# Kernel tuning notes

Hardware: AMD Instinct MI355X
Metric: run time of the kernel (lower is better)

## Reference

```python
import jax, jax.numpy as jnp
import numpy as np

K_CHEB = 3  # Chebyshev order K -> K+1 basis matrices, gcn order = K


def setup_inputs() -> dict:
    key = jax.random.key(0)
    ks = jax.random.split(key, 7)
    B, N, T, Cin, Cout, ndim = 32, 512, 12, 64, 64, 40
    support_len = K_CHEB + 1
    cin_total = (K_CHEB * support_len + 1) * Cin  # (order*support_len+1)*c_in = 832
    x = jax.random.normal(ks[0], (B, N, T, Cin), jnp.float32)
    adj = (jax.random.uniform(ks[1], (N, N)) < 0.05).astype(jnp.float32)
    adjacency = jnp.maximum(adj, jnp.eye(N, dtype=jnp.float32))
    embedding = jax.random.uniform(ks[2], (N, ndim), dtype=jnp.float32)  # nn.init.uniform_
    W1 = jax.random.normal(ks[3], (ndim, ndim // 2), jnp.float32) * 0.3
    W2 = jax.random.normal(ks[4], (ndim, ndim // 2), jnp.float32) * 0.3
    mlp_w = jax.random.normal(ks[5], (Cout, cin_total), jnp.float32) / np.float32(np.sqrt(cin_total))
    mlp_b = jnp.zeros((Cout,), jnp.float32)
    return {"x": x, "adjacency": adjacency, "embedding": embedding,
            "W1": W1, "W2": W2, "mlp_w": mlp_w, "mlp_b": mlp_b}


def _cheb_kernels(adjacency, embedding, W1, W2):
    # adaptive adjacency: embedding mixed through column-softmaxed projections
    e1 = embedding @ jax.nn.softmax(W1, axis=0)
    e2 = embedding @ jax.nn.softmax(W2, axis=0)
    e1 = e1 / (jnp.linalg.norm(e1, axis=1, keepdims=True) + 1e-8)
    e2 = e2 / (jnp.linalg.norm(e2, axis=1, keepdims=True) + 1e-8)
    weight = e1 @ e2.T  # (N, N)
    A = jnp.where(adjacency > 0.0, weight + adjacency, jnp.asarray(9e-15, adjacency.dtype))
    # symmetric normalization: L = I - D^-1/2 A D^-1/2 ; Ls = (2/maxeig)*L - I with maxeig=2 -> Ls = -sym(A)
    d = 1.0 / jnp.sqrt(A.sum(axis=1))
    Ls = -(d[:, None] * A * d[None, :])
    I = jnp.eye(A.shape[0], dtype=A.dtype)
    kernels = [I, Ls]
    for _ in range(1, K_CHEB):  # Chebyshev recursion: T_{k+1} = 2 Ls T_k - T_{k-1}
        kernels.append(2.0 * (Ls @ kernels[-1]) - kernels[-2])
    return kernels  # K_CHEB + 1 matrices of (N, N)


def reference(x, adjacency, embedding, W1, W2, mlp_w, mlp_b):
    supports = _cheb_kernels(adjacency, embedding, W1, W2)
    xp = jnp.transpose(x, (0, 3, 1, 2))  # (B, Cin, N, T)
    out = [xp]
    for a in supports:
        x1 = jnp.einsum('bcvt,vw->bcwt', xp, a)
        out.append(x1)
        for _ in range(2, K_CHEB + 1):  # gcn order = K_CHEB
            x1 = jnp.einsum('bcvt,vw->bcwt', x1, a)
            out.append(x1)
    h = jnp.concatenate(out, axis=1)  # (B, 832, N, T)
    h = jnp.einsum('bcvt,oc->bovt', h, mlp_w) + mlp_b[None, :, None, None]  # 1x1 conv
    h = jnp.transpose(h, (0, 2, 3, 1))  # (B, N, T, Cout)
    return jax.nn.relu(h + x)  # conv_r is None (Cin == Cout), dropout eval no-op
```

## Files before the change

### kernel.cpp

```cpp
#include <hip/hip_runtime.h>
#include <hip/hip_bf16.h>

typedef unsigned short ushortT;
typedef unsigned int uintT;
typedef __attribute__((ext_vector_type(8))) short bf16x8;
typedef __attribute__((ext_vector_type(4))) float f32x4;
typedef __attribute__((ext_vector_type(4))) unsigned short us4;
typedef __attribute__((ext_vector_type(8))) unsigned short us8;

__device__ __forceinline__ ushortT f2bf(float f) {
    union { float f; uintT u; } x; x.f = f;
    uintT r = x.u + 0x7fffu + ((x.u >> 16) & 1u);
    return (ushortT)(r >> 16);
}
__device__ __forceinline__ float bf2f(ushortT u) {
    union { uintT u; float f; } x; x.u = ((uintT)u) << 16; return x.f;
}

#define ZLD 260
#define KTOT 5120

__global__ __launch_bounds__(256) void k_embed(const float* __restrict__ emb,
                                               const float* __restrict__ W1,
                                               const float* __restrict__ W2,
                                               float* __restrict__ e1,
                                               float* __restrict__ e2) {
    __shared__ float sW[800];
    __shared__ float sWs[800];
    const float* W = (blockIdx.x == 0) ? W1 : W2;
    float* e = (blockIdx.x == 0) ? e1 : e2;
    int tid = threadIdx.x;
    for (int i = tid; i < 800; i += 256) sW[i] = W[i];
    __syncthreads();
    if (tid < 20) {
        float mx = -1e30f;
        for (int i = 0; i < 40; ++i) mx = fmaxf(mx, sW[i * 20 + tid]);
        float s = 0.f;
        for (int i = 0; i < 40; ++i) s += __expf(sW[i * 20 + tid] - mx);
        float inv = 1.f / s;
        for (int i = 0; i < 40; ++i) sWs[i * 20 + tid] = __expf(sW[i * 20 + tid] - mx) * inv;
    }
    __syncthreads();
    for (int row = tid; row < 512; row += 256) {
        float acc[20];
        #pragma unroll
        for (int j = 0; j < 20; ++j) acc[j] = 0.f;
        for (int i = 0; i < 40; ++i) {
            float ev = emb[row * 40 + i];
            #pragma unroll
            for (int j = 0; j < 20; ++j) acc[j] += ev * sWs[i * 20 + j];
        }
        float s = 0.f;
        #pragma unroll
        for (int j = 0; j < 20; ++j) s += acc[j] * acc[j];
        float scale = 1.f / (sqrtf(s) + 1e-8f);
        #pragma unroll
        for (int j = 0; j < 20; ++j) e[row * 20 + j] = acc[j] * scale;
    }
}

__global__ __launch_bounds__(256) void k_adj(const float* __restrict__ adj,
                                             const float* __restrict__ e1,
                                             const float* __restrict__ e2,
                                             float* __restrict__ A,
                                             float* __restrict__ d) {
    int v = blockIdx.x, tid = threadIdx.x;
    __shared__ float ev[20];
    if (tid < 20) ev[tid] = e1[v * 20 + tid];
    __syncthreads();
    float local = 0.f;
    for (int w = tid; w < 512; w += 256) {
        float dot = 0.f;
        #pragma unroll
        for (int j = 0; j < 20; ++j) dot += ev[j] * e2[w * 20 + j];
        float av = adj[v * 512 + w];
        float Av = (av > 0.f) ? (dot + av) : 9e-15f;
        A[v * 512 + w] = Av;
        local += Av;
    }
    __shared__ float red[256];
    red[tid] = local;
    __syncthreads();
    for (int s = 128; s > 0; s >>= 1) {
        if (tid < s) red[tid] += red[tid + s];
        __syncthreads();
    }
    if (tid == 0) d[v] = 1.f / sqrtf(red[0]);
}

__global__ __launch_bounds__(256) void k_m(const float* __restrict__ A,
                                           const float* __restrict__ d,
                                           ushortT* __restrict__ P) {
    int w = blockIdx.x, tid = threadIdx.x;
    float dw = d[w];
    for (int v = tid; v < 512; v += 256) {
        float val = -d[v] * dw * A[v * 512 + w];
        P[512 * 512 + w * 512 + v] = f2bf(val);
        P[w * 512 + v] = (v == w) ? (ushortT)0x3F80 : (ushortT)0;
    }
}

__global__ __launch_bounds__(256) void k_w(const float* __restrict__ mlp_w,
                                           ushortT* __restrict__ Wq) {
    int idx = blockIdx.x * 256 + threadIdx.x;
    if (idx >= 10 * 64 * 64) return;
    int q = idx >> 12, rem = idx & 4095, o = rem >> 6, c = rem & 63;
    float v;
    if (q == 0) {
        v = 0.f;
        #pragma unroll
        for (int k = 0; k < 4; ++k) v += mlp_w[o * 832 + k * 64 + c];
    } else {
        v = mlp_w[o * 832 + (q + 3) * 64 + c];
    }
    Wq[idx] = f2bf(v);
}

__global__ __launch_bounds__(256) void k_gemm512(const ushortT* __restrict__ A,
                                                 const ushortT* __restrict__ B,
                                                 ushortT* __restrict__ out1,
                                                 ushortT* __restrict__ out2,
                                                 int mode,
                                                 const ushortT* __restrict__ aux,
                                                 const ushortT* __restrict__ A2,
                                                 const ushortT* __restrict__ B2,
                                                 ushortT* __restrict__ out3) {
    int bx = blockIdx.x;
    if (bx >= 64) { A = A2; B = B2; out1 = out3; out2 = nullptr; mode = 0; bx -= 64; }
    int wave = threadIdx.x >> 6, lane = threadIdx.x & 63;
    int lr = lane & 15, lg = lane >> 4;
    int mbase = (bx >> 3) * 64;
    int nbase = (bx & 7) * 64 + wave * 16;
    f32x4 acc[4] = {};
    for (int kk = 0; kk < 16; ++kk) {
        int k0 = kk * 32 + lg * 8;
        bf16x8 bfr;
        #pragma unroll
        for (int j = 0; j < 8; ++j) bfr[j] = (short)B[(k0 + j) * 512 + nbase + lr];
        #pragma unroll
        for (int wt = 0; wt < 4; ++wt) {
            bf16x8 af = *(const bf16x8*)(A + (mbase + wt * 16 + lr) * 512 + k0);
            acc[wt] = __builtin_amdgcn_mfma_f32_16x16x32_bf16(af, bfr, acc[wt], 0, 0, 0);
        }
    }
    #pragma unroll
    for (int wt = 0; wt < 4; ++wt)
        #pragma unroll
        for (int r = 0; r < 4; ++r) {
            int row = mbase + wt * 16 + lg * 4 + r;
            int col = nbase + lr;
            float v = acc[wt][r];
            out1[row * 512 + col] = f2bf(v);
            if (mode == 1) out2[row * 512 + col] = f2bf(2.f * v - (row == col ? 1.f : 0.f));
            else if (mode == 2) out2[row * 512 + col] = f2bf(4.f * v - 3.f * bf2f(aux[row * 512 + col]));
        }
}

__global__ __launch_bounds__(256) void k_z(const float* __restrict__ x,
                                           const ushortT* __restrict__ Wq,
                                           ushortT* __restrict__ Z,
                                           int slab0) {
    __shared__ ushortT Zl[64 * ZLD];
    int bid = blockIdx.x;
    int btl = bid >> 1, chunk = bid & 1;
    int bt = slab0 + btl;
    int b = bt / 12, t = bt - b * 12;
    int tid = threadIdx.x, wave = tid >> 6, lane = tid & 63;
    int lr = lane & 15, lg = lane >> 4;

    bf16x8 xn[4][2];
    const float* xb = x + ((size_t)b * 512 * 12 + t) * 64;
    #pragma unroll
    for (int vt = 0; vt < 4; ++vt) {
        int vrow = chunk * 256 + wave * 64 + vt * 16 + lr;
        const float* px = xb + (size_t)vrow * 768 + lg * 8;
        f32x4 f0 = *(const f32x4*)px;
        f32x4 f1 = *(const f32x4*)(px + 4);
        f32x4 f2 = *(const f32x4*)(px + 32);
        f32x4 f3 = *(const f32x4*)(px + 36);
        bf16x8 v0, v1;
        v0[0] = (short)f2bf(f0[0]); v0[1] = (short)f2bf(f0[1]);
        v0[2] = (short)f2bf(f0[2]); v0[3] = (short)f2bf(f0[3]);
        v0[4] = (short)f2bf(f1[0]); v0[5] = (short)f2bf(f1[1]);
        v0[6] = (short)f2bf(f1[2]); v0[7] = (short)f2bf(f1[3]);
        v1[0] = (short)f2bf(f2[0]); v1[1] = (short)f2bf(f2[1]);
        v1[2] = (short)f2bf(f2[2]); v1[3] = (short)f2bf(f2[3]);
        v1[4] = (short)f2bf(f3[0]); v1[5] = (short)f2bf(f3[1]);
        v1[6] = (short)f2bf(f3[2]); v1[7] = (short)f2bf(f3[3]);
        xn[vt][0] = v0;
        xn[vt][1] = v1;
    }

    #pragma unroll 1
    for (int q = 0; q < 10; ++q) {
        const ushortT* wqp = Wq + q * 4096;
        #pragma unroll
        for (int ot = 0; ot < 4; ++ot) {
            int o = ot * 16 + lr;
            bf16x8 wf0 = *(const bf16x8*)(wqp + o * 64 + lg * 8);
            bf16x8 wf1 = *(const bf16x8*)(wqp + o * 64 + 32 + lg * 8);
            #pragma unroll
            for (int vt = 0; vt < 4; ++vt) {
                f32x4 z = {};
                z = __builtin_amdgcn_mfma_f32_16x16x32_bf16(xn[vt][0], wf0, z, 0, 0, 0);
                z = __builtin_amdgcn_mfma_f32_16x16x32_bf16(xn[vt][1], wf1, z, 0, 0, 0);
                us4 pk = { f2bf(z[0]), f2bf(z[1]), f2bf(z[2]), f2bf(z[3]) };
                *(us4*)&Zl[o * ZLD + wave * 64 + vt * 16 + lg * 4] = pk;
            }
        }
        __syncthreads();
        size_t kbase = (size_t)q * 512 + chunk * 256;
        #pragma unroll
        for (int j = 0; j < 8; ++j) {
            int flat = j * 256 + tid;
            int o = flat >> 5, slot = flat & 31;
            us4 lo = *(const us4*)&Zl[o * ZLD + slot * 8];
            us4 hi = *(const us4*)&Zl[o * ZLD + slot * 8 + 4];
            us8 val = { lo[0], lo[1], lo[2], lo[3], hi[0], hi[1], hi[2], hi[3] };
            *(us8*)&Z[(size_t)(btl * 64 + o) * KTOT + kbase + slot * 8] = val;
        }
        __syncthreads();
    }
}

__global__ __launch_bounds__(256) void k_big(const ushortT* __restrict__ P,
                                             const ushortT* __restrict__ Z,
                                             const float* __restrict__ x,
                                             const float* __restrict__ bias,
                                             float* __restrict__ out,
                                             int slab0) {
    __shared__ ushortT SA[3][4096];
    __shared__ ushortT SB[3][4096];
    int nwg = (int)gridDim.x;
    int bid = (int)blockIdx.x;
    int cpx = nwg >> 3;
    int lbid = (bid & 7) * cpx + (bid >> 3);
    int mblk = lbid & 3;
    int nblk = lbid >> 2;
    int mbase = mblk * 128;
    int n0 = nblk * 128;
    int tid = threadIdx.x, wave = tid >> 6, lane = tid & 63;
    int lr = lane & 15, lg = lane >> 4;
    int wm = wave >> 1, wn = wave & 1;
    int srow = tid >> 2, sg = tid & 3;

    f32x4 acc[4][4] = {};

    auto stage = [&](int kt, int buf) {
        int q = kt >> 4;
        int v0 = (kt & 15) * 32;
        const ushortT* Pk = P + (size_t)q * 262144 + v0 + sg * 8;
        const ushortT* Zk = Z + (size_t)kt * 32 + sg * 8;
        #pragma unroll
        for (int i = 0; i < 2; ++i) {
            int row = i * 64 + srow;
            __builtin_amdgcn_global_load_lds(Pk + (size_t)(mbase + row) * 512,
                                             &SA[buf][(i * 256 + wave * 64) * 8], 16, 0, 0);
            __builtin_amdgcn_global_load_lds(Zk + (size_t)(n0 + row) * KTOT,
                                             &SB[buf][(i * 256 + wave * 64) * 8], 16, 0, 0);
        }
    };

    auto phase = [&](int kt, int wsel) {
        if (wsel == 0)      asm volatile("s_waitcnt vmcnt(8)" ::: "memory");
        else if (wsel == 1) asm volatile("s_waitcnt vmcnt(4)" ::: "memory");
        else                asm volatile("s_waitcnt vmcnt(0)" ::: "memory");
        __builtin_amdgcn_sched_barrier(0);
        __builtin_amdgcn_s_barrier();
        __builtin_amdgcn_sched_barrier(0);
        int buf = kt % 3;
        bf16x8 af[4], bfr[4];
        #pragma unroll
        for (int mt = 0; mt < 4; ++mt) {
            int m = wm * 64 + mt * 16 + lr;
            af[mt] = *(const bf16x8*)&SA[buf][m * 32 + lg * 8];
        }
        #pragma unroll
        for (int nt = 0; nt < 4; ++nt) {
            int n = wn * 64 + nt * 16 + lr;
            bfr[nt] = *(const bf16x8*)&SB[buf][n * 32 + lg * 8];
        }
        __builtin_amdgcn_s_setprio(1);
        #pragma unroll
        for (int mt = 0; mt < 4; ++mt)
            #pragma unroll
            for (int nt = 0; nt < 4; ++nt)
                acc[mt][nt] = __builtin_amdgcn_mfma_f32_16x16x32_bf16(af[mt], bfr[nt], acc[mt][nt], 0, 0, 0);
        __builtin_amdgcn_s_setprio(0);
        __builtin_amdgcn_sched_barrier(0);
        __builtin_amdgcn_s_barrier();
        __builtin_amdgcn_sched_barrier(0);
        if (kt + 3 < 160) stage(kt + 3, (kt + 3) % 3);
    };

    stage(0, 0);
    __builtin_amdgcn_sched_barrier(0);
    stage(1, 1);
    __builtin_amdgcn_sched_barrier(0);
    stage(2, 2);
    __builtin_amdgcn_sched_barrier(0);

    #pragma unroll 1
    for (int kt = 0; kt < 158; ++kt) phase(kt, 0);
    phase(158, 1);
    phase(159, 2);

    #pragma unroll
    for (int mt = 0; mt < 4; ++mt)
        #pragma unroll
        for (int nt = 0; nt < 4; ++nt)
            #pragma unroll
            for (int r = 0; r < 4; ++r) {
                int m = mbase + wm * 64 + mt * 16 + lg * 4 + r;
                int nf = n0 + wn * 64 + nt * 16 + lr;
                int btl = nf >> 6, o = nf & 63;
                int bt = slab0 + btl;
                int bb = bt / 12, t = bt - bb * 12;
                size_t oi = (((size_t)bb * 512 + m) * 12 + t) * 64 + o;
                float v = acc[mt][nt][r] + x[oi] + bias[o];
                out[oi] = (v > 0.f) ? v : 0.f;
            }
}

__global__ __launch_bounds__(256, 2) void k_main_fb(const float* __restrict__ x,
                                                    const ushortT* __restrict__ P,
                                                    const ushortT* __restrict__ Wq,
                                                    const float* __restrict__ bias,
                                                    float* __restrict__ out) {
    __shared__ ushortT Zt[64 * ZLD];
    const int SZ = 512 * 512;
    int bid = blockIdx.x;
    int slot = bid & 7, idx = bid >> 3;
    int half = slot >> 2;
    int bt = idx * 4 + (slot & 3);
    int b = bt / 12, tt = bt - b * 12;
    int tid = threadIdx.x, wave = tid >> 6, lane = tid & 63;
    int lr = lane & 15, lg = lane >> 4;
    int wbase = half * 256 + wave * 64;
    int vzb = wave * 64;
    const float* xqf = x + ((size_t)b * 512 * 12 + tt) * 64;

    f32x4 oacc[4][4] = {};
    bf16x8 xn[4][2];

    auto xload = [&](int ch) {
        #pragma unroll
        for (int vt = 0; vt < 4; ++vt) {
            int vrow = ch * 256 + vzb + vt * 16 + lr;
            const float* px = xqf + (size_t)vrow * 768 + lg * 8;
            f32x4 f0 = *(const f32x4*)px;
            f32x4 f1 = *(const f32x4*)(px + 4);
            f32x4 f2 = *(const f32x4*)(px + 32);
            f32x4 f3 = *(const f32x4*)(px + 36);
            bf16x8 v0, v1;
            v0[0] = (short)f2bf(f0[0]); v0[1] = (short)f2bf(f0[1]);
            v0[2] = (short)f2bf(f0[2]); v0[3] = (short)f2bf(f0[3]);
            v0[4] = (short)f2bf(f1[0]); v0[5] = (short)f2bf(f1[1]);
            v0[6] = (short)f2bf(f1[2]); v0[7] = (short)f2bf(f1[3]);
            v1[0] = (short)f2bf(f2[0]); v1[1] = (short)f2bf(f2[1]);
            v1[2] = (short)f2bf(f2[2]); v1[3] = (short)f2bf(f2[3]);
            v1[4] = (short)f2bf(f3[0]); v1[5] = (short)f2bf(f3[1]);
            v1[6] = (short)f2bf(f3[2]); v1[7] = (short)f2bf(f3[3]);
            xn[vt][0] = v0;
            xn[vt][1] = v1;
        }
    };
    auto zphase = [&](int q) {
        const ushortT* wqp = Wq + q * 4096;
        #pragma unroll
        for (int vt = 0; vt < 4; ++vt)
            #pragma unroll
            for (int ot = 0; ot < 4; ++ot) {
                int o = ot * 16 + lr;
                bf16x8 wf0 = *(const bf16x8*)(wqp + o * 64 + lg * 8);
                bf16x8 wf1 = *(const bf16x8*)(wqp + o * 64 + 32 + lg * 8);
                f32x4 z = {};
                z = __builtin_amdgcn_mfma_f32_16x16x32_bf16(xn[vt][0], wf0, z, 0, 0, 0);
                z = __builtin_amdgcn_mfma_f32_16x16x32_bf16(xn[vt][1], wf1, z, 0, 0, 0);
                us4 pk = { f2bf(z[0]), f2bf(z[1]), f2bf(z[2]), f2bf(z[3]) };
                *(us4*)&Zt[o * ZLD + vzb + vt * 16 + lg * 4] = pk;
            }
    };
    auto pptr = [&](int j, int mt) -> const ushortT* {
        int q = 1 + (j >> 1), ch = j & 1;
        return P + (size_t)q * SZ + (size_t)(wbase + mt * 16 + lr) * 512 + ch * 256 + lg * 8;
    };

    xload(half);
    zphase(0);
    xload(0);
    __syncthreads();
    #pragma unroll
    for (int mt = 0; mt < 4; ++mt)
        #pragma unroll
        for (int ot = 0; ot < 4; ++ot) {
            int o = ot * 16 + lr;
            us4 z4 = *(const us4*)&Zt[o * ZLD + wave * 64 + mt * 16 + lg * 4];
            oacc[mt][ot][0] = bf2f(z4[0]);
            oacc[mt][ot][1] = bf2f(z4[1]);
            oacc[mt][ot][2] = bf2f(z4[2]);
            oacc[mt][ot][3] = bf2f(z4[3]);
        }
    __syncthreads();

    #pragma unroll 1
    for (int j = 0; j < 18; ++j) {
        int q = 1 + (j >> 1);
        zphase(q);
        int jn = (j < 17) ? j + 1 : 17;
        xload(jn & 1);
        __syncthreads();
        const ushortT* pc0 = pptr(j, 0);
        const ushortT* pc1 = pptr(j, 1);
        const ushortT* pc2 = pptr(j, 2);
        const ushortT* pc3 = pptr(j, 3);
        #pragma unroll
        for (int kk = 0; kk < 8; ++kk) {
            bf16x8 a0 = *(const bf16x8*)(pc0 + kk * 32);
            bf16x8 a1 = *(const bf16x8*)(pc1 + kk * 32);
            bf16x8 a2 = *(const bf16x8*)(pc2 + kk * 32);
            bf16x8 a3 = *(const bf16x8*)(pc3 + kk * 32);
            int vb = kk * 32 + lg * 8;
            bf16x8 b0 = *(const bf16x8*)&Zt[(0 * 16 + lr) * ZLD + vb];
            bf16x8 b1 = *(const bf16x8*)&Zt[(1 * 16 + lr) * ZLD + vb];
            bf16x8 b2 = *(const bf16x8*)&Zt[(2 * 16 + lr) * ZLD + vb];
            bf16x8 b3 = *(const bf16x8*)&Zt[(3 * 16 + lr) * ZLD + vb];
            oacc[0][0] = __builtin_amdgcn_mfma_f32_16x16x32_bf16(a0, b0, oacc[0][0], 0, 0, 0);
            oacc[1][0] = __builtin_amdgcn_mfma_f32_16x16x32_bf16(a1, b0, oacc[1][0], 0, 0, 0);
            oacc[2][0] = __builtin_amdgcn_mfma_f32_16x16x32_bf16(a2, b0, oacc[2][0], 0, 0, 0);
            oacc[3][0] = __builtin_amdgcn_mfma_f32_16x16x32_bf16(a3, b0, oacc[3][0], 0, 0, 0);
            oacc[0][1] = __builtin_amdgcn_mfma_f32_16x16x32_bf16(a0, b1, oacc[0][1], 0, 0, 0);
            oacc[1][1] = __builtin_amdgcn_mfma_f32_16x16x32_bf16(a1, b1, oacc[1][1], 0, 0, 0);
            oacc[2][1] = __builtin_amdgcn_mfma_f32_16x16x32_bf16(a2, b1, oacc[2][1], 0, 0, 0);
            oacc[3][1] = __builtin_amdgcn_mfma_f32_16x16x32_bf16(a3, b1, oacc[3][1], 0, 0, 0);
            oacc[0][2] = __builtin_amdgcn_mfma_f32_16x16x32_bf16(a0, b2, oacc[0][2], 0, 0, 0);
            oacc[1][2] = __builtin_amdgcn_mfma_f32_16x16x32_bf16(a1, b2, oacc[1][2], 0, 0, 0);
            oacc[2][2] = __builtin_amdgcn_mfma_f32_16x16x32_bf16(a2, b2, oacc[2][2], 0, 0, 0);
            oacc[3][2] = __builtin_amdgcn_mfma_f32_16x16x32_bf16(a3, b2, oacc[3][2], 0, 0, 0);
            oacc[0][3] = __builtin_amdgcn_mfma_f32_16x16x32_bf16(a0, b3, oacc[0][3], 0, 0, 0);
            oacc[1][3] = __builtin_amdgcn_mfma_f32_16x16x32_bf16(a1, b3, oacc[1][3], 0, 0, 0);
            oacc[2][3] = __builtin_amdgcn_mfma_f32_16x16x32_bf16(a2, b3, oacc[2][3], 0, 0, 0);
            oacc[3][3] = __builtin_amdgcn_mfma_f32_16x16x32_bf16(a3, b3, oacc[3][3], 0, 0, 0);
        }
        __syncthreads();
    }

    #pragma unroll
    for (int mt = 0; mt < 4; ++mt)
        #pragma unroll
        for (int ot = 0; ot < 4; ++ot)
            #pragma unroll
            for (int r = 0; r < 4; ++r) {
                int w = wbase + mt * 16 + lg * 4 + r;
                int o = ot * 16 + lr;
                size_t oi = (((size_t)b * 512 + w) * 12 + tt) * 64 + o;
                float v = oacc[mt][ot][r] + x[oi] + bias[o];
                out[oi] = (v > 0.f) ? v : 0.f;
            }
}

extern "C" void kernel_launch(void* const* d_in, const int* in_sizes, int n_in,
                              void* d_out, int out_size, void* d_ws, size_t ws_size,
                              hipStream_t stream) {
    const float* x    = (const float*)d_in[0];
    const float* adj  = (const float*)d_in[1];
    const float* emb  = (const float*)d_in[2];
    const float* W1   = (const float*)d_in[3];
    const float* W2   = (const float*)d_in[4];
    const float* mlpw = (const float*)d_in[5];
    const float* mlpb = (const float*)d_in[6];
    float* out = (float*)d_out;

    char* ws = (char*)d_ws;
    float*   e1   = (float*)(ws + 0);
    float*   e2   = (float*)(ws + 65536);
    float*   A    = (float*)(ws + 131072);
    float*   dvec = (float*)(ws + 1179648);
    ushortT* P    = (ushortT*)(ws + 1183744);
    ushortT* Wq   = (ushortT*)(ws + 6426624);
    ushortT* Z    = (ushortT*)(ws + 6508544);
    const size_t ZOFF = 6508544;

    k_embed<<<2, 256, 0, stream>>>(emb, W1, W2, e1, e2);
    k_adj<<<512, 256, 0, stream>>>(adj, e1, e2, A, dvec);
    k_m<<<512, 256, 0, stream>>>(A, dvec, P);
    k_w<<<160, 256, 0, stream>>>(mlpw, Wq);

    const int SZ = 512 * 512;
    ushortT *S1 = P + 1 * SZ, *S2 = P + 2 * SZ, *S3 = P + 3 * SZ, *S4 = P + 4 * SZ,
            *S5 = P + 5 * SZ, *S6 = P + 6 * SZ, *S7 = P + 7 * SZ, *S8 = P + 8 * SZ,
            *S9 = P + 9 * SZ;
    k_gemm512<<<64, 256, 0, stream>>>(S1, S1, S2, S4, 1, nullptr, nullptr, nullptr, nullptr);
    k_gemm512<<<128, 256, 0, stream>>>(S1, S2, S3, S7, 2, S1, S4, S4, S5);
    k_gemm512<<<128, 256, 0, stream>>>(S4, S5, S6, nullptr, 0, nullptr, S7, S7, S8);
    k_gemm512<<<64, 256, 0, stream>>>(S7, S8, S9, nullptr, 0, nullptr, nullptr, nullptr, nullptr);

    const size_t ZFULL = (size_t)24576 * KTOT * 2;
    int nslab = 1;
    while (nslab <= 8 && ws_size < ZOFF + ZFULL / (size_t)nslab) nslab <<= 1;

    if (nslab <= 8) {
        int btps = 384 / nslab;
        for (int s = 0; s < nslab; ++s) {
            k_z<<<btps * 2, 256, 0, stream>>>(x, Wq, Z, s * btps);
            k_big<<<btps * 2, 256, 0, stream>>>(P, Z, x, mlpb, out, s * btps);
        }
    } else {
        k_main_fb<<<768, 256, 0, stream>>>(x, P, Wq, mlpb, out);
    }
    (void)in_sizes; (void)n_in; (void)out_size;
}
```

Before: 327.2 us.

## Restructure main GEMM pipeline to one barrier per k-step and fuse setup kernels

```diff
diff --git a/kernel.cpp b/kernel.cpp
--- a/kernel.cpp
+++ b/kernel.cpp
@@ -90,30 +90,32 @@
 
 __global__ __launch_bounds__(256) void k_m(const float* __restrict__ A,
                                            const float* __restrict__ d,
-                                           ushortT* __restrict__ P) {
-    int w = blockIdx.x, tid = threadIdx.x;
-    float dw = d[w];
-    for (int v = tid; v < 512; v += 256) {
-        float val = -d[v] * dw * A[v * 512 + w];
-        P[512 * 512 + w * 512 + v] = f2bf(val);
-        P[w * 512 + v] = (v == w) ? (ushortT)0x3F80 : (ushortT)0;
-    }
-}
-
-__global__ __launch_bounds__(256) void k_w(const float* __restrict__ mlp_w,
+                                           ushortT* __restrict__ P,
+                                           const float* __restrict__ mlp_w,
                                            ushortT* __restrict__ Wq) {
-    int idx = blockIdx.x * 256 + threadIdx.x;
-    if (idx >= 10 * 64 * 64) return;
-    int q = idx >> 12, rem = idx & 4095, o = rem >> 6, c = rem & 63;
-    float v;
-    if (q == 0) {
-        v = 0.f;
-        #pragma unroll
-        for (int k = 0; k < 4; ++k) v += mlp_w[o * 832 + k * 64 + c];
+    int bx = blockIdx.x, tid = threadIdx.x;
+    if (bx < 512) {
+        int w = bx;
+        float dw = d[w];
+        for (int v = tid; v < 512; v += 256) {
+            float val = -d[v] * dw * A[v * 512 + w];
+            P[512 * 512 + w * 512 + v] = f2bf(val);
+            P[w * 512 + v] = (v == w) ? (ushortT)0x3F80 : (ushortT)0;
+        }
     } else {
-        v = mlp_w[o * 832 + (q + 3) * 64 + c];
-    }
-    Wq[idx] = f2bf(v);
+        int idx = (bx - 512) * 256 + tid;
+        if (idx >= 10 * 64 * 64) return;
+        int q = idx >> 12, rem = idx & 4095, o = rem >> 6, c = rem & 63;
+        float v;
+        if (q == 0) {
+            v = 0.f;
+            #pragma unroll
+            for (int k = 0; k < 4; ++k) v += mlp_w[o * 832 + k * 64 + c];
+        } else {
+            v = mlp_w[o * 832 + (q + 3) * 64 + c];
+        }
+        Wq[idx] = f2bf(v);
+    }
 }
 
 __global__ __launch_bounds__(256) void k_gemm512(const ushortT* __restrict__ A,
@@ -261,13 +263,7 @@
         }
     };
 
-    auto phase = [&](int kt, int wsel) {
-        if (wsel == 0)      asm volatile("s_waitcnt vmcnt(8)" ::: "memory");
-        else if (wsel == 1) asm volatile("s_waitcnt vmcnt(4)" ::: "memory");
-        else                asm volatile("s_waitcnt vmcnt(0)" ::: "memory");
-        __builtin_amdgcn_sched_barrier(0);
-        __builtin_amdgcn_s_barrier();
-        __builtin_amdgcn_sched_barrier(0);
+    auto phase = [&](int kt) {
         int buf = kt % 3;
         bf16x8 af[4], bfr[4];
         #pragma unroll
@@ -280,6 +276,10 @@
             int n = wn * 64 + nt * 16 + lr;
             bfr[nt] = *(const bf16x8*)&SB[buf][n * 32 + lg * 8];
         }
+        bool more = (kt + 2 < 160);
+        if (more) stage(kt + 2, (kt + 2) % 3);
+        asm volatile("s_waitcnt lgkmcnt(0)" ::: "memory");
+        __builtin_amdgcn_sched_barrier(0);
         __builtin_amdgcn_s_setprio(1);
         #pragma unroll
         for (int mt = 0; mt < 4; ++mt)
@@ -288,22 +288,22 @@
                 acc[mt][nt] = __builtin_amdgcn_mfma_f32_16x16x32_bf16(af[mt], bfr[nt], acc[mt][nt], 0, 0, 0);
         __builtin_amdgcn_s_setprio(0);
         __builtin_amdgcn_sched_barrier(0);
+        if (more) asm volatile("s_waitcnt vmcnt(4)" ::: "memory");
+        else      asm volatile("s_waitcnt vmcnt(0)" ::: "memory");
+        __builtin_amdgcn_sched_barrier(0);
         __builtin_amdgcn_s_barrier();
         __builtin_amdgcn_sched_barrier(0);
-        if (kt + 3 < 160) stage(kt + 3, (kt + 3) % 3);
     };
 
     stage(0, 0);
+    stage(1, 1);
+    asm volatile("s_waitcnt vmcnt(0)" ::: "memory");
     __builtin_amdgcn_sched_barrier(0);
-    stage(1, 1);
+    __builtin_amdgcn_s_barrier();
     __builtin_amdgcn_sched_barrier(0);
-    stage(2, 2);
-    __builtin_amdgcn_sched_barrier(0);
 
     #pragma unroll 1
-    for (int kt = 0; kt < 158; ++kt) phase(kt, 0);
-    phase(158, 1);
-    phase(159, 2);
+    for (int kt = 0; kt < 160; ++kt) phase(kt);
 
     #pragma unroll
     for (int mt = 0; mt < 4; ++mt)
@@ -483,8 +483,7 @@
 
     k_embed<<<2, 256, 0, stream>>>(emb, W1, W2, e1, e2);
     k_adj<<<512, 256, 0, stream>>>(adj, e1, e2, A, dvec);
-    k_m<<<512, 256, 0, stream>>>(A, dvec, P);
-    k_w<<<160, 256, 0, stream>>>(mlpw, Wq);
+    k_m<<<672, 256, 0, stream>>>(A, dvec, P, mlpw, Wq);
 
     const int SZ = 512 * 512;
     ushortT *S1 = P + 1 * SZ, *S2 = P + 2 * SZ, *S3 = P + 3 * SZ, *S4 = P + 4 * SZ,
```

After: 373.0 us. +14.0%, slower.

## Fuse k_m with k_w and overlap Z precompute with Chebyshev GEMM launches

Applied to the files above, without the earlier changes.

```diff
diff --git a/kernel.cpp b/kernel.cpp
--- a/kernel.cpp
+++ b/kernel.cpp
@@ -90,79 +90,40 @@
 
 __global__ __launch_bounds__(256) void k_m(const float* __restrict__ A,
                                            const float* __restrict__ d,
-                                           ushortT* __restrict__ P) {
-    int w = blockIdx.x, tid = threadIdx.x;
-    float dw = d[w];
-    for (int v = tid; v < 512; v += 256) {
-        float val = -d[v] * dw * A[v * 512 + w];
-        P[512 * 512 + w * 512 + v] = f2bf(val);
-        P[w * 512 + v] = (v == w) ? (ushortT)0x3F80 : (ushortT)0;
-    }
-}
-
-__global__ __launch_bounds__(256) void k_w(const float* __restrict__ mlp_w,
+                                           ushortT* __restrict__ P,
+                                           const float* __restrict__ mlp_w,
                                            ushortT* __restrict__ Wq) {
-    int idx = blockIdx.x * 256 + threadIdx.x;
-    if (idx >= 10 * 64 * 64) return;
-    int q = idx >> 12, rem = idx & 4095, o = rem >> 6, c = rem & 63;
-    float v;
-    if (q == 0) {
-        v = 0.f;
-        #pragma unroll
-        for (int k = 0; k < 4; ++k) v += mlp_w[o * 832 + k * 64 + c];
+    int bx = blockIdx.x, tid = threadIdx.x;
+    if (bx < 512) {
+        int w = bx;
+        float dw = d[w];
+        for (int v = tid; v < 512; v += 256) {
+            float val = -d[v] * dw * A[v * 512 + w];
+            P[512 * 512 + w * 512 + v] = f2bf(val);
+            P[w * 512 + v] = (v == w) ? (ushortT)0x3F80 : (ushortT)0;
+        }
     } else {
-        v = mlp_w[o * 832 + (q + 3) * 64 + c];
-    }
-    Wq[idx] = f2bf(v);
-}
-
-__global__ __launch_bounds__(256) void k_gemm512(const ushortT* __restrict__ A,
-                                                 const ushortT* __restrict__ B,
-                                                 ushortT* __restrict__ out1,
-                                                 ushortT* __restrict__ out2,
-                                                 int mode,
-                                                 const ushortT* __restrict__ aux,
-                                                 const ushortT* __restrict__ A2,
-                                                 const ushortT* __restrict__ B2,
-                                                 ushortT* __restrict__ out3) {
-    int bx = blockIdx.x;
-    if (bx >= 64) { A = A2; B = B2; out1 = out3; out2 = nullptr; mode = 0; bx -= 64; }
-    int wave = threadIdx.x >> 6, lane = threadIdx.x & 63;
-    int lr = lane & 15, lg = lane >> 4;
-    int mbase = (bx >> 3) * 64;
-    int nbase = (bx & 7) * 64 + wave * 16;
-    f32x4 acc[4] = {};
-    for (int kk = 0; kk < 16; ++kk) {
-        int k0 = kk * 32 + lg * 8;
-        bf16x8 bfr;
-        #pragma unroll
-        for (int j = 0; j < 8; ++j) bfr[j] = (short)B[(k0 + j) * 512 + nbase + lr];
-        #pragma unroll
-        for (int wt = 0; wt < 4; ++wt) {
-            bf16x8 af = *(const bf16x8*)(A + (mbase + wt * 16 + lr) * 512 + k0);
-            acc[wt] = __builtin_amdgcn_mfma_f32_16x16x32_bf16(af, bfr, acc[wt], 0, 0, 0);
-        }
-    }
-    #pragma unroll
-    for (int wt = 0; wt < 4; ++wt)
-        #pragma unroll
-        for (int r = 0; r < 4; ++r) {
-            int row = mbase + wt * 16 + lg * 4 + r;
-            int col = nbase + lr;
-            float v = acc[wt][r];
-            out1[row * 512 + col] = f2bf(v);
-            if (mode == 1) out2[row * 512 + col] = f2bf(2.f * v - (row == col ? 1.f : 0.f));
-            else if (mode == 2) out2[row * 512 + col] = f2bf(4.f * v - 3.f * bf2f(aux[row * 512 + col]));
-        }
-}
-
-__global__ __launch_bounds__(256) void k_z(const float* __restrict__ x,
-                                           const ushortT* __restrict__ Wq,
-                                           ushortT* __restrict__ Z,
-                                           int slab0) {
+        int idx = (bx - 512) * 256 + tid;
+        if (idx >= 10 * 64 * 64) return;
+        int q = idx >> 12, rem = idx & 4095, o = rem >> 6, c = rem & 63;
+        float v;
+        if (q == 0) {
+            v = 0.f;
+            #pragma unroll
+            for (int k = 0; k < 4; ++k) v += mlp_w[o * 832 + k * 64 + c];
+        } else {
+            v = mlp_w[o * 832 + (q + 3) * 64 + c];
+        }
+        Wq[idx] = f2bf(v);
+    }
+}
+
+__device__ void kz_body(const float* __restrict__ x,
+                        const ushortT* __restrict__ Wq,
+                        ushortT* __restrict__ Z,
+                        int kzbid, int slab0) {
     __shared__ ushortT Zl[64 * ZLD];
-    int bid = blockIdx.x;
-    int btl = bid >> 1, chunk = bid & 1;
+    int btl = kzbid >> 1, chunk = kzbid & 1;
     int bt = slab0 + btl;
     int b = bt / 12, t = bt - b * 12;
     int tid = threadIdx.x, wave = tid >> 6, lane = tid & 63;
@@ -221,6 +182,61 @@
         }
         __syncthreads();
     }
+}
+
+__global__ __launch_bounds__(256) void k_z(const float* __restrict__ x,
+                                           const ushortT* __restrict__ Wq,
+                                           ushortT* __restrict__ Z,
+                                           int slab0) {
+    kz_body(x, Wq, Z, blockIdx.x, slab0);
+}
+
+__global__ __launch_bounds__(256) void k_gemm512(const ushortT* __restrict__ A,
+                                                 const ushortT* __restrict__ B,
+                                                 ushortT* __restrict__ out1,
+                                                 ushortT* __restrict__ out2,
+                                                 int mode,
+                                                 const ushortT* __restrict__ aux,
+                                                 const ushortT* __restrict__ A2,
+                                                 const ushortT* __restrict__ B2,
+                                                 ushortT* __restrict__ out3,
+                                                 const float* __restrict__ x,
+                                                 const ushortT* __restrict__ Wq,
+                                                 ushortT* __restrict__ Z,
+                                                 int kz_start, int kz_part) {
+    int bx = blockIdx.x;
+    if (bx >= kz_start) {
+        kz_body(x, Wq, Z, (bx - kz_start) + kz_part * 192, 0);
+        return;
+    }
+    if (bx >= 64) { A = A2; B = B2; out1 = out3; out2 = nullptr; mode = 0; bx -= 64; }
+    int wave = threadIdx.x >> 6, lane = threadIdx.x & 63;
+    int lr = lane & 15, lg = lane >> 4;
+    int mbase = (bx >> 3) * 64;
+    int nbase = (bx & 7) * 64 + wave * 16;
+    f32x4 acc[4] = {};
+    for (int kk = 0; kk < 16; ++kk) {
+        int k0 = kk * 32 + lg * 8;
+        bf16x8 bfr;
+        #pragma unroll
+        for (int j = 0; j < 8; ++j) bfr[j] = (short)B[(k0 + j) * 512 + nbase + lr];
+        #pragma unroll
+        for (int wt = 0; wt < 4; ++wt) {
+            bf16x8 af = *(const bf16x8*)(A + (mbase + wt * 16 + lr) * 512 + k0);
+            acc[wt] = __builtin_amdgcn_mfma_f32_16x16x32_bf16(af, bfr, acc[wt], 0, 0, 0);
+        }
+    }
+    #pragma unroll
+    for (int wt = 0; wt < 4; ++wt)
+        #pragma unroll
+        for (int r = 0; r < 4; ++r) {
+            int row = mbase + wt * 16 + lg * 4 + r;
+            int col = nbase + lr;
+            float v = acc[wt][r];
+            out1[row * 512 + col] = f2bf(v);
+            if (mode == 1) out2[row * 512 + col] = f2bf(2.f * v - (row == col ? 1.f : 0.f));
+            else if (mode == 2) out2[row * 512 + col] = f2bf(4.f * v - 3.f * bf2f(aux[row * 512 + col]));
+        }
 }
 
 __global__ __launch_bounds__(256) void k_big(const ushortT* __restrict__ P,
@@ -483,23 +499,43 @@
 
     k_embed<<<2, 256, 0, stream>>>(emb, W1, W2, e1, e2);
     k_adj<<<512, 256, 0, stream>>>(adj, e1, e2, A, dvec);
-    k_m<<<512, 256, 0, stream>>>(A, dvec, P);
-    k_w<<<160, 256, 0, stream>>>(mlpw, Wq);
+    k_m<<<672, 256, 0, stream>>>(A, dvec, P, mlpw, Wq);
 
     const int SZ = 512 * 512;
     ushortT *S1 = P + 1 * SZ, *S2 = P + 2 * SZ, *S3 = P + 3 * SZ, *S4 = P + 4 * SZ,
             *S5 = P + 5 * SZ, *S6 = P + 6 * SZ, *S7 = P + 7 * SZ, *S8 = P + 8 * SZ,
             *S9 = P + 9 * SZ;
-    k_gemm512<<<64, 256, 0, stream>>>(S1, S1, S2, S4, 1, nullptr, nullptr, nullptr, nullptr);
-    k_gemm512<<<128, 256, 0, stream>>>(S1, S2, S3, S7, 2, S1, S4, S4, S5);
-    k_gemm512<<<128, 256, 0, stream>>>(S4, S5, S6, nullptr, 0, nullptr, S7, S7, S8);
-    k_gemm512<<<64, 256, 0, stream>>>(S7, S8, S9, nullptr, 0, nullptr, nullptr, nullptr, nullptr);
 
     const size_t ZFULL = (size_t)24576 * KTOT * 2;
     int nslab = 1;
     while (nslab <= 8 && ws_size < ZOFF + ZFULL / (size_t)nslab) nslab <<= 1;
-
-    if (nslab <= 8) {
+    const int BIG = 1 << 30;
+
+    if (nslab == 1) {
+        k_gemm512<<<256, 256, 0, stream>>>(S1, S1, S2, S4, 1, nullptr,
+                                           nullptr, nullptr, nullptr,
+                                           x, Wq, Z, 64, 0);
+        k_gemm512<<<320, 256, 0, stream>>>(S1, S2, S3, S7, 2, S1,
+                                           S4, S4, S5,
+                                           x, Wq, Z, 128, 1);
+        k_gemm512<<<320, 256, 0, stream>>>(S4, S5, S6, nullptr, 0, nullptr,
+                                           S7, S7, S8,
+                                           x, Wq, Z, 128, 2);
+        k_gemm512<<<256, 256, 0, stream>>>(S7, S8, S9, nullptr, 0, nullptr,
+                                           nullptr, nullptr, nullptr,
+                                           x, Wq, Z, 64, 3);
+        k_big<<<768, 256, 0, stream>>>(P, Z, x, mlpb, out, 0);
+    } else if (nslab <= 8) {
+        k_gemm512<<<64, 256, 0, stream>>>(S1, S1, S2, S4, 1, nullptr,
+                                          nullptr, nullptr, nullptr,
+                                          x, Wq, Z, BIG, 0);
+        k_gemm512<<<128, 256, 0, stream>>>(S1, S2, S3, S7, 2, S1,
+                                           S4, S4, S5, x, Wq, Z, BIG, 0);
+        k_gemm512<<<128, 256, 0, stream>>>(S4, S5, S6, nullptr, 0, nullptr,
+                                           S7, S7, S8, x, Wq, Z, BIG, 0);
+        k_gemm512<<<64, 256, 0, stream>>>(S7, S8, S9, nullptr, 0, nullptr,
+                                          nullptr, nullptr, nullptr,
+                                          x, Wq, Z, BIG, 0);
         int btps = 384 / nslab;
         for (int s = 0; s < nslab; ++s) {
             k_z<<<btps * 2, 256, 0, stream>>>(x, Wq, Z, s * btps);
```

Result: slower. 360.1 us (+10.1%).
